# Optimization experiments

Hardware: AMD Instinct MI355X
Metric: run time of the kernel (lower is better)

The kernel has to match this reference:

```python
import jax, jax.numpy as jnp
import numpy as np

B, S, D, H = 4, 2048, 1024, 16
HD = D // H  # head_dim = 64
SCALE = HD ** -0.5


def setup_inputs() -> dict:
    key = jax.random.key(0)
    k1, k2, k3, k4, k5 = jax.random.split(key, 5)
    std = D ** -0.5
    return {
        "x": jax.random.normal(k1, (B, S, D), dtype=jnp.float32),
        "w_qkv": jax.random.normal(k2, (D, 3 * D), dtype=jnp.float32) * std,
        "b_qkv": jax.random.normal(k3, (3 * D,), dtype=jnp.float32) * 0.01,
        "w_out": jax.random.normal(k4, (D, D), dtype=jnp.float32) * std,
        "b_out": jax.random.normal(k5, (D,), dtype=jnp.float32) * 0.01,
    }


def reference(x, w_qkv, b_qkv, w_out, b_out):
    b, s, d = x.shape
    qkv = x @ w_qkv + b_qkv                                   # [B,S,3D]
    qkv = qkv.reshape(b, s, 3, H, HD).transpose(2, 0, 3, 1, 4)  # [3,B,H,S,HD]
    q, k, v = qkv[0], qkv[1], qkv[2]
    attn = jnp.einsum("bhqd,bhkd->bhqk", q, k) * SCALE        # [B,H,S,S]
    attn = jax.nn.softmax(attn, axis=-1)
    out = jnp.einsum("bhqk,bhkd->bhqd", attn, v)              # [B,H,S,HD]
    out = out.transpose(0, 2, 1, 3).reshape(b, s, d)          # [B,S,D]
    return out @ w_out + b_out
```

## Files before the change

kernel.cpp:

```cpp
#include <hip/hip_runtime.h>
#include <stdint.h>
#include <stddef.h>

#define NB 4
#define NS 2048
#define ND 1024
#define NH 16
#define HDIM 64
#define SCALE 0.125f
#define CLOG2E 0.18033688011112042f

typedef __attribute__((ext_vector_type(4))) float f32x4;
typedef __attribute__((ext_vector_type(16))) float f32x16;
typedef __attribute__((ext_vector_type(8))) __bf16 bf16x8;
typedef __attribute__((ext_vector_type(4))) uint32_t u32x4;

__device__ __forceinline__ uint16_t f2bf(float f) {
  uint32_t u = __builtin_bit_cast(uint32_t, f);
  return (uint16_t)((u + 0x7fffu + ((u >> 16) & 1u)) >> 16);
}

__device__ __forceinline__ void gload_lds16(const void* g, void* l) {
  __builtin_amdgcn_global_load_lds((const __attribute__((address_space(1))) void*)g,
                                   (__attribute__((address_space(3))) void*)l, 16, 0, 0);
}

__device__ __forceinline__ uint32_t cvtpk(float lo, float hi) {
  uint32_t r;
  asm("v_cvt_pk_bf16_f32 %0, %1, %2" : "=v"(r) : "v"(lo), "v"(hi));
  return r;
}

__device__ __forceinline__ void permswap(uint32_t& a, uint32_t& b) {
  asm("v_permlane32_swap_b32 %0, %1" : "+v"(a), "+v"(b));
}

__device__ __forceinline__ float fexp2(float x) {
  float r;
  asm("v_exp_f32 %0, %1" : "=v"(r) : "v"(x));
  return r;
}

__global__ __launch_bounds__(256)
void k_prep(const float* __restrict__ x, const float* __restrict__ wq,
            const float* __restrict__ wo, uint16_t* __restrict__ Xb,
            uint16_t* __restrict__ Wq, uint16_t* __restrict__ Wo) {
  __shared__ float tile[64][65];
  const int bid = blockIdx.x, tid = threadIdx.x;
  if (bid < 8192) {
    int i = bid * 256 + tid;
    float4 v = reinterpret_cast<const float4*>(x)[i];
    ushort4 o;
    o.x = f2bf(v.x); o.y = f2bf(v.y); o.z = f2bf(v.z); o.w = f2bf(v.w);
    reinterpret_cast<ushort4*>(Xb)[i] = o;
    return;
  }
  const float* in; uint16_t* out; int K, N, bx, by;
  if (bid < 8960) { int r = bid - 8192; in = wq; out = Wq; K = 1024; N = 3072; bx = r % 48; by = r / 48; }
  else            { int r = bid - 8960; in = wo; out = Wo; K = 1024; N = 1024; bx = r % 16; by = r / 16; }
  const int nb = bx * 64, kb = by * 64;
  const int c = tid & 63, r0 = tid >> 6;
#pragma unroll
  for (int i = 0; i < 16; ++i) {
    int r = r0 * 16 + i;
    tile[r][c] = in[(size_t)(kb + r) * N + nb + c];
  }
  __syncthreads();
#pragma unroll
  for (int i = 0; i < 16; ++i) {
    int rr = r0 * 16 + i;
    out[(size_t)(nb + rr) * K + kb + c] = f2bf(tile[c][rr]);
  }
}

__global__ __launch_bounds__(512)
void k_gemm256(const uint16_t* __restrict__ A, const uint16_t* __restrict__ Bt,
               const float* __restrict__ bias, uint16_t* __restrict__ C,
               uint16_t* __restrict__ vt, int M, int N, int K) {
  __shared__ __align__(16) char Al[2][32768];
  __shared__ __align__(16) char Bl[2][32768];
  const int tid = threadIdx.x, wave = tid >> 6, lane = tid & 63;

  const int flat = blockIdx.y * gridDim.x + blockIdx.x;
  const int cpx = (gridDim.x * gridDim.y) >> 3;
  const int swz = (flat & 7) * cpx + (flat >> 3);
  const int bx = swz % gridDim.x, by = swz / gridDim.x;
  const int mb = by * 256, nb = bx * 256;

  const int wm = wave >> 2, wn = wave & 3;
  const int fr = lane & 15, cc = lane >> 4;
  f32x4 acc[8][4] = {};
  const int NT = K >> 6;
  const int sslot = tid & 7;

#define STAGE(BUF, KT) do {                                                     \
    const int kb_ = (KT) * 64;                                                  \
    _Pragma("unroll")                                                           \
    for (int i = 0; i < 4; ++i) {                                               \
      int row = (i * 512 + tid) >> 3;                                           \
      int ch = sslot ^ (row & 7);                                               \
      gload_lds16(A + (size_t)(mb + row) * K + kb_ + ch * 8,                    \
                  Al[BUF] + (size_t)(i * 512 + (wave << 6)) * 16);              \
    }                                                                           \
    _Pragma("unroll")                                                           \
    for (int i = 0; i < 4; ++i) {                                               \
      int row = (i * 512 + tid) >> 3;                                           \
      int ch = sslot ^ (row & 7);                                               \
      gload_lds16(Bt + (size_t)(nb + row) * K + kb_ + ch * 8,                   \
                  Bl[BUF] + (size_t)(i * 512 + (wave << 6)) * 16);              \
    }                                                                           \
  } while (0)

  STAGE(0, 0);
  asm volatile("s_waitcnt vmcnt(0)" ::: "memory");
  __builtin_amdgcn_s_barrier();

  for (int kt = 0; kt < NT; ++kt) {
    const int cur = kt & 1;
    const bool issue = (kt + 1 < NT);
    if (issue) STAGE(cur ^ 1, kt + 1);

#pragma unroll
    for (int ks = 0; ks < 2; ++ks) {
      bf16x8 af[8], bfg[4];
#pragma unroll
      for (int i = 0; i < 8; ++i) {
        int ra = wm * 128 + i * 16 + fr;
        af[i] = *(const bf16x8*)(Al[cur] + ra * 128 + (((ks * 4 + cc) ^ (ra & 7)) * 16));
      }
#pragma unroll
      for (int j = 0; j < 4; ++j) {
        int rb = wn * 64 + j * 16 + fr;
        bfg[j] = *(const bf16x8*)(Bl[cur] + rb * 128 + (((ks * 4 + cc) ^ (rb & 7)) * 16));
      }
      __builtin_amdgcn_s_setprio(1);
#pragma unroll
      for (int i = 0; i < 8; ++i)
#pragma unroll
        for (int j = 0; j < 4; ++j)
          acc[i][j] = __builtin_amdgcn_mfma_f32_16x16x32_bf16(af[i], bfg[j], acc[i][j], 0, 0, 0);
      __builtin_amdgcn_s_setprio(0);
    }

    if (issue) {
      asm volatile("s_waitcnt vmcnt(0)" ::: "memory");
      __builtin_amdgcn_s_barrier();
    }
  }
#undef STAGE

  if (nb < 2048) {
    const float qs = (nb < 1024) ? CLOG2E : 1.0f;
#pragma unroll
    for (int i = 0; i < 8; ++i)
#pragma unroll
      for (int j = 0; j < 4; ++j)
#pragma unroll
        for (int r = 0; r < 4; ++r) {
          int row = mb + wm * 128 + i * 16 + cc * 4 + r;
          int col = nb + wn * 64 + j * 16 + fr;
          C[(size_t)row * N + col] = f2bf((acc[i][j][r] + bias[col]) * qs);
        }
  } else {
    const int b_ = mb >> 11;
    const int h_ = ((nb - 2048) >> 6) + wn;
    const int s0 = (mb & 2047) + wm * 128;
    uint16_t* vb = vt + (size_t)(b_ * 16 + h_) * 64 * NS;
#pragma unroll
    for (int i = 0; i < 8; ++i)
#pragma unroll
      for (int j = 0; j < 4; ++j) {
        int col = nb + wn * 64 + j * 16 + fr;
        int d = j * 16 + fr;
        float bcol = bias[col];
        ushort4 o;
        o.x = f2bf(acc[i][j][0] + bcol);
        o.y = f2bf(acc[i][j][1] + bcol);
        o.z = f2bf(acc[i][j][2] + bcol);
        o.w = f2bf(acc[i][j][3] + bcol);
        int s = s0 + i * 16 + cc * 4;
        *reinterpret_cast<ushort4*>(vb + (size_t)d * NS + s) = o;
      }
  }
}

template<int OUT_BF16>
__global__ __launch_bounds__(256)
void k_gemm(const uint16_t* __restrict__ A, const uint16_t* __restrict__ Bt,
            const float* __restrict__ bias, void* __restrict__ C,
            int M, int N, int K) {
  __shared__ __align__(16) char Al[8192];
  __shared__ __align__(16) char Bl[8192];
  const int tid = threadIdx.x;
  const int wave = tid >> 6, lane = tid & 63;
  const int mb = blockIdx.y * 128, nb = blockIdx.x * 128;
  const int wm = (wave >> 1) * 64, wn = (wave & 1) * 64;
  const int fr = lane & 15, cc = lane >> 4;
  const int srow = tid >> 2, sch = tid & 3;
  f32x4 acc[4][4] = {};

  for (int kb = 0; kb < K; kb += 32) {
#pragma unroll
    for (int p = 0; p < 2; ++p) {
      int row = p * 64 + srow;
      int cg = sch ^ (row & 3) ^ ((row >> 2) & 3);
      gload_lds16(A + (size_t)(mb + row) * K + kb + cg * 8, Al + p * 4096 + wave * 1024);
      gload_lds16(Bt + (size_t)(nb + row) * K + kb + cg * 8, Bl + p * 4096 + wave * 1024);
    }
    __syncthreads();
    bf16x8 af[4], bfr[4];
#pragma unroll
    for (int i = 0; i < 4; ++i) {
      int ra = wm + i * 16 + fr;
      af[i] = *(const bf16x8*)(Al + ra * 64 + ((cc ^ (ra & 3) ^ ((ra >> 2) & 3)) * 16));
      int rb = wn + i * 16 + fr;
      bfr[i] = *(const bf16x8*)(Bl + rb * 64 + ((cc ^ (rb & 3) ^ ((rb >> 2) & 3)) * 16));
    }
#pragma unroll
    for (int i = 0; i < 4; ++i)
#pragma unroll
      for (int j = 0; j < 4; ++j)
        acc[i][j] = __builtin_amdgcn_mfma_f32_16x16x32_bf16(af[i], bfr[j], acc[i][j], 0, 0, 0);
    __syncthreads();
  }

#pragma unroll
  for (int i = 0; i < 4; ++i)
#pragma unroll
    for (int j = 0; j < 4; ++j)
#pragma unroll
      for (int r = 0; r < 4; ++r) {
        int row = mb + wm + i * 16 + cc * 4 + r;
        int col = nb + wn + j * 16 + fr;
        float v = acc[i][j][r] + bias[col];
        if (OUT_BF16)
          ((uint16_t*)C)[(size_t)row * N + col] = f2bf(v);
        else
          ((float*)C)[(size_t)row * N + col] = v;
      }
}

__global__ __launch_bounds__(256)
void k_attn(const uint16_t* __restrict__ qkv, const uint16_t* __restrict__ vt,
            uint16_t* __restrict__ out) {
  __shared__ __align__(16) char Kl[2][8192];
  __shared__ __align__(16) char Vl[2][8192];

  const int id = blockIdx.y * 16 + blockIdx.x;
  const int wfid = (id & 7) * 128 + (id >> 3);
  const int bh = wfid >> 4, qblk = wfid & 15;
  const int b = bh >> 4, h = bh & 15;
  const int tid = threadIdx.x, wave = tid >> 6, lane = tid & 63;
  const int ln31 = lane & 31, hi = lane >> 5;

  const int q0 = qblk * 128 + wave * 32;
  const uint16_t* qrowp = qkv + (size_t)(b * NS + q0 + ln31) * 3072 + h * 64 + hi * 8;
  bf16x8 qf[4];
#pragma unroll
  for (int kk = 0; kk < 4; ++kk) qf[kk] = *(const bf16x8*)(qrowp + kk * 16);

  const int srow = tid >> 3;
  const int cs = (tid & 7) ^ (srow & 7);
  const uint16_t* ksrc = qkv + (size_t)(b * NS) * 3072 + 1024 + h * 64 + cs * 8;
  const uint16_t* vsrc = vt + (size_t)bh * 64 * NS + cs * 8;

  f32x16 acc0 = {}, acc1 = {};
  float l_run = 0.f;

#pragma unroll
  for (int r = 0; r < 2; ++r) {
    int row = srow + r * 32;
    gload_lds16(ksrc + (size_t)row * 3072, Kl[0] + wave * 1024 + r * 4096);
    gload_lds16(vsrc + (size_t)row * NS, Vl[0] + wave * 1024 + r * 4096);
  }
  asm volatile("s_waitcnt vmcnt(0)" ::: "memory");
  __builtin_amdgcn_s_barrier();
  __builtin_amdgcn_sched_barrier(0);

  const int ksw = ln31 & 7;

  for (int t = 0; t < NS / 64; ++t) {
    const int cur = t & 1;
    if (t < NS / 64 - 1) {
      const int kb2 = (t + 1) * 64;
      char* kd = Kl[cur ^ 1] + wave * 1024;
      char* vd = Vl[cur ^ 1] + wave * 1024;
#pragma unroll
      for (int r = 0; r < 2; ++r) {
        int row = srow + r * 32;
        gload_lds16(ksrc + (size_t)(kb2 + row) * 3072, kd + r * 4096);
        gload_lds16(vsrc + (size_t)row * NS + kb2, vd + r * 4096);
      }
      asm volatile("s_waitcnt vmcnt(4)" ::: "memory");
    } else {
      asm volatile("s_waitcnt vmcnt(0)" ::: "memory");
    }
    __builtin_amdgcn_s_barrier();
    __builtin_amdgcn_sched_barrier(0);

    const char* kb0 = Kl[cur] + ln31 * 128;
    const char* kb1 = kb0 + 32 * 128;
    f32x16 st0 = {}, st1 = {};
    __builtin_amdgcn_s_setprio(1);
#pragma unroll
    for (int kk = 0; kk < 4; ++kk) {
      int c = ((kk * 2 + hi) ^ ksw) * 16;
      bf16x8 k0 = *(const bf16x8*)(kb0 + c);
      bf16x8 k1 = *(const bf16x8*)(kb1 + c);
      st0 = __builtin_amdgcn_mfma_f32_32x32x16_bf16(k0, qf[kk], st0, 0, 0, 0);
      st1 = __builtin_amdgcn_mfma_f32_32x32x16_bf16(k1, qf[kk], st1, 0, 0, 0);
    }
    __builtin_amdgcn_s_setprio(0);

    float rs = 0.f;
#pragma unroll
    for (int r = 0; r < 16; ++r) { st0[r] = fexp2(st0[r]); rs += st0[r]; }
#pragma unroll
    for (int r = 0; r < 16; ++r) { st1[r] = fexp2(st1[r]); rs += st1[r]; }
    l_run += rs;

    const char* vb0 = Vl[cur] + ln31 * 128;
    const char* vb1 = vb0 + 32 * 128;
    __builtin_amdgcn_s_setprio(1);
#pragma unroll
    for (int h2 = 0; h2 < 2; ++h2) {
      f32x16 ph = h2 ? st1 : st0;
#pragma unroll
      for (int s2 = 0; s2 < 2; ++s2) {
        const int kkp = h2 * 2 + s2;
        const int s8 = s2 * 8;
        uint32_t A0 = cvtpk(ph[s8 + 0], ph[s8 + 1]);
        uint32_t A1 = cvtpk(ph[s8 + 2], ph[s8 + 3]);
        uint32_t B0 = cvtpk(ph[s8 + 4], ph[s8 + 5]);
        uint32_t B1 = cvtpk(ph[s8 + 6], ph[s8 + 7]);
        permswap(A0, B0);
        permswap(A1, B1);
        u32x4 pw = {A0, A1, B0, B1};
        bf16x8 pf = __builtin_bit_cast(bf16x8, pw);
        int c = ((kkp * 2 + hi) ^ ksw) * 16;
        bf16x8 v0 = *(const bf16x8*)(vb0 + c);
        bf16x8 v1 = *(const bf16x8*)(vb1 + c);
        acc0 = __builtin_amdgcn_mfma_f32_32x32x16_bf16(v0, pf, acc0, 0, 0, 0);
        acc1 = __builtin_amdgcn_mfma_f32_32x32x16_bf16(v1, pf, acc1, 0, 0, 0);
      }
    }
    __builtin_amdgcn_s_setprio(0);

    __builtin_amdgcn_s_barrier();
  }

  const float rl = 1.0f / (l_run + __shfl_xor(l_run, 32));
  char* sc = (char*)Kl + wave * 4096 + ln31 * 128;
  const int qsw = ln31 & 15;
#pragma unroll
  for (int dn = 0; dn < 2; ++dn) {
    f32x16 a = dn ? acc1 : acc0;
#pragma unroll
    for (int g = 0; g < 4; ++g) {
      uint2 w;
      w.x = cvtpk(a[4 * g + 0] * rl, a[4 * g + 1] * rl);
      w.y = cvtpk(a[4 * g + 2] * rl, a[4 * g + 3] * rl);
      int c8 = (dn * 8 + 2 * g + hi) ^ qsw;
      *(uint2*)(sc + c8 * 8) = w;
    }
  }
  char* outp = (char*)out + ((size_t)(b * NS + q0 + ln31) * 1024 + h * 64 + hi * 32) * 2;
#pragma unroll
  for (int cc2 = 0; cc2 < 4; ++cc2) {
    uint2 va = *(const uint2*)(sc + (((hi * 8 + 2 * cc2 + 0) ^ qsw) * 8));
    uint2 vb2 = *(const uint2*)(sc + (((hi * 8 + 2 * cc2 + 1) ^ qsw) * 8));
    u32x4 o = {va.x, va.y, vb2.x, vb2.y};
    *(u32x4*)(outp + cc2 * 16) = o;
  }
}

extern "C" void kernel_launch(void* const* d_in, const int* in_sizes, int n_in,
                              void* d_out, int out_size, void* d_ws, size_t ws_size,
                              hipStream_t stream) {
  const float* x     = (const float*)d_in[0];
  const float* w_qkv = (const float*)d_in[1];
  const float* b_qkv = (const float*)d_in[2];
  const float* w_out = (const float*)d_in[3];
  const float* b_out = (const float*)d_in[4];
  float* out = (float*)d_out;
  char* ws = (char*)d_ws;

  uint16_t* Xb    = (uint16_t*)(ws);
  uint16_t* Wqkvt = (uint16_t*)(ws + (16u << 20));
  uint16_t* Woutt = (uint16_t*)(ws + (22u << 20));
  uint16_t* QKV   = (uint16_t*)(ws + (24u << 20));
  uint16_t* Vt    = (uint16_t*)(ws + (72u << 20));
  uint16_t* AO    = Xb;

  k_prep<<<9216, 256, 0, stream>>>(x, w_qkv, w_out, Xb, Wqkvt, Woutt);
  k_gemm256<<<dim3(12, 32), 512, 0, stream>>>(Xb, Wqkvt, b_qkv, QKV, Vt, NB * NS, 3 * ND, ND);
  k_attn<<<dim3(16, 64), 256, 0, stream>>>(QKV, Vt, AO);
  k_gemm<0><<<dim3(8, 64), 256, 0, stream>>>(AO, Woutt, b_out, out, NB * NS, ND, ND);
}
```

Measured before the change: 211.2 us.

## Replace 256x256 double-buffered QKV GEMM with simpler 128x128 single-buffer kernel

Swaps the 512-thread 256x256-tile QKV projection GEMM (double-buffered LDS, 64-wide K steps, grid swizzle, setprio) for a 256-thread 128x128-tile kernel with 32-wide K steps, a single LDS buffer and two barriers per iteration. The grid grows from 384 to 1536 blocks, which gives more blocks per CU and lower LDS use. In exchange it loses load/compute overlap inside a block, the L2-friendly swizzle and the per-tile reuse of the larger tile.

After: 223.9 us. +6.0%, slower.

```diff
diff --git a/kernel.cpp b/kernel.cpp
--- a/kernel.cpp
+++ b/kernel.cpp
@@ -73,104 +73,67 @@
   }
 }
 
-__global__ __launch_bounds__(512)
-void k_gemm256(const uint16_t* __restrict__ A, const uint16_t* __restrict__ Bt,
-               const float* __restrict__ bias, uint16_t* __restrict__ C,
-               uint16_t* __restrict__ vt, int M, int N, int K) {
-  __shared__ __align__(16) char Al[2][32768];
-  __shared__ __align__(16) char Bl[2][32768];
-  const int tid = threadIdx.x, wave = tid >> 6, lane = tid & 63;
-
-  const int flat = blockIdx.y * gridDim.x + blockIdx.x;
-  const int cpx = (gridDim.x * gridDim.y) >> 3;
-  const int swz = (flat & 7) * cpx + (flat >> 3);
-  const int bx = swz % gridDim.x, by = swz / gridDim.x;
-  const int mb = by * 256, nb = bx * 256;
-
-  const int wm = wave >> 2, wn = wave & 3;
+__global__ __launch_bounds__(256)
+void k_gemm1(const uint16_t* __restrict__ A, const uint16_t* __restrict__ Bt,
+             const float* __restrict__ bias, uint16_t* __restrict__ C,
+             uint16_t* __restrict__ vt, int M, int N, int K) {
+  __shared__ __align__(16) char Al[8192];
+  __shared__ __align__(16) char Bl[8192];
+  const int tid = threadIdx.x;
+  const int wave = tid >> 6, lane = tid & 63;
+  const int mb = blockIdx.y * 128, nb = blockIdx.x * 128;
+  const int wm = (wave >> 1) * 64, wn = (wave & 1) * 64;
   const int fr = lane & 15, cc = lane >> 4;
-  f32x4 acc[8][4] = {};
-  const int NT = K >> 6;
-  const int sslot = tid & 7;
-
-#define STAGE(BUF, KT) do {                                                     \
-    const int kb_ = (KT) * 64;                                                  \
-    _Pragma("unroll")                                                           \
-    for (int i = 0; i < 4; ++i) {                                               \
-      int row = (i * 512 + tid) >> 3;                                           \
-      int ch = sslot ^ (row & 7);                                               \
-      gload_lds16(A + (size_t)(mb + row) * K + kb_ + ch * 8,                    \
-                  Al[BUF] + (size_t)(i * 512 + (wave << 6)) * 16);              \
-    }                                                                           \
-    _Pragma("unroll")                                                           \
-    for (int i = 0; i < 4; ++i) {                                               \
-      int row = (i * 512 + tid) >> 3;                                           \
-      int ch = sslot ^ (row & 7);                                               \
-      gload_lds16(Bt + (size_t)(nb + row) * K + kb_ + ch * 8,                   \
-                  Bl[BUF] + (size_t)(i * 512 + (wave << 6)) * 16);              \
-    }                                                                           \
-  } while (0)
-
-  STAGE(0, 0);
-  asm volatile("s_waitcnt vmcnt(0)" ::: "memory");
-  __builtin_amdgcn_s_barrier();
-
-  for (int kt = 0; kt < NT; ++kt) {
-    const int cur = kt & 1;
-    const bool issue = (kt + 1 < NT);
-    if (issue) STAGE(cur ^ 1, kt + 1);
-
-#pragma unroll
-    for (int ks = 0; ks < 2; ++ks) {
-      bf16x8 af[8], bfg[4];
-#pragma unroll
-      for (int i = 0; i < 8; ++i) {
-        int ra = wm * 128 + i * 16 + fr;
-        af[i] = *(const bf16x8*)(Al[cur] + ra * 128 + (((ks * 4 + cc) ^ (ra & 7)) * 16));
-      }
-#pragma unroll
-      for (int j = 0; j < 4; ++j) {
-        int rb = wn * 64 + j * 16 + fr;
-        bfg[j] = *(const bf16x8*)(Bl[cur] + rb * 128 + (((ks * 4 + cc) ^ (rb & 7)) * 16));
-      }
-      __builtin_amdgcn_s_setprio(1);
-#pragma unroll
-      for (int i = 0; i < 8; ++i)
-#pragma unroll
-        for (int j = 0; j < 4; ++j)
-          acc[i][j] = __builtin_amdgcn_mfma_f32_16x16x32_bf16(af[i], bfg[j], acc[i][j], 0, 0, 0);
-      __builtin_amdgcn_s_setprio(0);
-    }
-
-    if (issue) {
-      asm volatile("s_waitcnt vmcnt(0)" ::: "memory");
-      __builtin_amdgcn_s_barrier();
-    }
-  }
-#undef STAGE
+  const int srow = tid >> 2, sch = tid & 3;
+  f32x4 acc[4][4] = {};
+
+  for (int kb = 0; kb < K; kb += 32) {
+#pragma unroll
+    for (int p = 0; p < 2; ++p) {
+      int row = p * 64 + srow;
+      int cg = sch ^ (row & 3) ^ ((row >> 2) & 3);
+      gload_lds16(A + (size_t)(mb + row) * K + kb + cg * 8, Al + p * 4096 + wave * 1024);
+      gload_lds16(Bt + (size_t)(nb + row) * K + kb + cg * 8, Bl + p * 4096 + wave * 1024);
+    }
+    __syncthreads();
+    bf16x8 af[4], bfr[4];
+#pragma unroll
+    for (int i = 0; i < 4; ++i) {
+      int ra = wm + i * 16 + fr;
+      af[i] = *(const bf16x8*)(Al + ra * 64 + ((cc ^ (ra & 3) ^ ((ra >> 2) & 3)) * 16));
+      int rb = wn + i * 16 + fr;
+      bfr[i] = *(const bf16x8*)(Bl + rb * 64 + ((cc ^ (rb & 3) ^ ((rb >> 2) & 3)) * 16));
+    }
+#pragma unroll
+    for (int i = 0; i < 4; ++i)
+#pragma unroll
+      for (int j = 0; j < 4; ++j)
+        acc[i][j] = __builtin_amdgcn_mfma_f32_16x16x32_bf16(af[i], bfr[j], acc[i][j], 0, 0, 0);
+    __syncthreads();
+  }
 
   if (nb < 2048) {
     const float qs = (nb < 1024) ? CLOG2E : 1.0f;
 #pragma unroll
-    for (int i = 0; i < 8; ++i)
+    for (int i = 0; i < 4; ++i)
 #pragma unroll
       for (int j = 0; j < 4; ++j)
 #pragma unroll
         for (int r = 0; r < 4; ++r) {
-          int row = mb + wm * 128 + i * 16 + cc * 4 + r;
-          int col = nb + wn * 64 + j * 16 + fr;
+          int row = mb + wm + i * 16 + cc * 4 + r;
+          int col = nb + wn + j * 16 + fr;
           C[(size_t)row * N + col] = f2bf((acc[i][j][r] + bias[col]) * qs);
         }
   } else {
     const int b_ = mb >> 11;
-    const int h_ = ((nb - 2048) >> 6) + wn;
-    const int s0 = (mb & 2047) + wm * 128;
+    const int h_ = ((nb - 2048) >> 6) + (wn >> 6);
+    const int s0 = (mb & 2047) + wm;
     uint16_t* vb = vt + (size_t)(b_ * 16 + h_) * 64 * NS;
 #pragma unroll
-    for (int i = 0; i < 8; ++i)
+    for (int i = 0; i < 4; ++i)
 #pragma unroll
       for (int j = 0; j < 4; ++j) {
-        int col = nb + wn * 64 + j * 16 + fr;
+        int col = nb + wn + j * 16 + fr;
         int d = j * 16 + fr;
         float bcol = bias[col];
         ushort4 o;
@@ -393,7 +356,7 @@
   uint16_t* AO    = Xb;
 
   k_prep<<<9216, 256, 0, stream>>>(x, w_qkv, w_out, Xb, Wqkvt, Woutt);
-  k_gemm256<<<dim3(12, 32), 512, 0, stream>>>(Xb, Wqkvt, b_qkv, QKV, Vt, NB * NS, 3 * ND, ND);
+  k_gemm1<<<dim3(24, 64), 256, 0, stream>>>(Xb, Wqkvt, b_qkv, QKV, Vt, NB * NS, 3 * ND, ND);
   k_attn<<<dim3(16, 64), 256, 0, stream>>>(QKV, Vt, AO);
   k_gemm<0><<<dim3(8, 64), 256, 0, stream>>>(AO, Woutt, b_out, out, NB * NS, ND, ND);
 }
```

## Load V fragments directly from global into registers instead of LDS staging

Applied to the files above, without the earlier changes.

Removes the LDS double buffer for V^T and has each lane load its V fragments for the current tile directly from global memory into registers at the top of each iteration. K staging through LDS is kept, and the vmcnt waits are adjusted to account for the eight extra outstanding vector loads. This cuts LDS traffic and capacity per block, which may raise occupancy. In exchange, each wave now fetches V redundantly, V loads get no prefetch distance beyond the QK^T and softmax phase, and global latency may be exposed.

Result: slower. 252.0 us (+19.3%).

```diff
diff --git a/kernel.cpp b/kernel.cpp
--- a/kernel.cpp
+++ b/kernel.cpp
@@ -244,7 +244,6 @@
 void k_attn(const uint16_t* __restrict__ qkv, const uint16_t* __restrict__ vt,
             uint16_t* __restrict__ out) {
   __shared__ __align__(16) char Kl[2][8192];
-  __shared__ __align__(16) char Vl[2][8192];
 
   const int id = blockIdx.y * 16 + blockIdx.x;
   const int wfid = (id & 7) * 128 + (id >> 3);
@@ -262,17 +261,14 @@
   const int srow = tid >> 3;
   const int cs = (tid & 7) ^ (srow & 7);
   const uint16_t* ksrc = qkv + (size_t)(b * NS) * 3072 + 1024 + h * 64 + cs * 8;
-  const uint16_t* vsrc = vt + (size_t)bh * 64 * NS + cs * 8;
+  const uint16_t* vrow0 = vt + (size_t)bh * 64 * NS + (size_t)ln31 * NS + hi * 8;
+  const uint16_t* vrow1 = vrow0 + (size_t)32 * NS;
 
   f32x16 acc0 = {}, acc1 = {};
   float l_run = 0.f;
 
-#pragma unroll
-  for (int r = 0; r < 2; ++r) {
-    int row = srow + r * 32;
-    gload_lds16(ksrc + (size_t)row * 3072, Kl[0] + wave * 1024 + r * 4096);
-    gload_lds16(vsrc + (size_t)row * NS, Vl[0] + wave * 1024 + r * 4096);
-  }
+  gload_lds16(ksrc + (size_t)srow * 3072, Kl[0] + wave * 1024);
+  gload_lds16(ksrc + (size_t)(srow + 32) * 3072, Kl[0] + wave * 1024 + 4096);
   asm volatile("s_waitcnt vmcnt(0)" ::: "memory");
   __builtin_amdgcn_s_barrier();
   __builtin_amdgcn_sched_barrier(0);
@@ -281,19 +277,22 @@
 
   for (int t = 0; t < NS / 64; ++t) {
     const int cur = t & 1;
+
+    bf16x8 vf0[4], vf1[4];
+#pragma unroll
+    for (int kkp = 0; kkp < 4; ++kkp) {
+      vf0[kkp] = *(const bf16x8*)(vrow0 + t * 64 + kkp * 16);
+      vf1[kkp] = *(const bf16x8*)(vrow1 + t * 64 + kkp * 16);
+    }
+
     if (t < NS / 64 - 1) {
       const int kb2 = (t + 1) * 64;
       char* kd = Kl[cur ^ 1] + wave * 1024;
-      char* vd = Vl[cur ^ 1] + wave * 1024;
-#pragma unroll
-      for (int r = 0; r < 2; ++r) {
-        int row = srow + r * 32;
-        gload_lds16(ksrc + (size_t)(kb2 + row) * 3072, kd + r * 4096);
-        gload_lds16(vsrc + (size_t)row * NS + kb2, vd + r * 4096);
-      }
-      asm volatile("s_waitcnt vmcnt(4)" ::: "memory");
+      gload_lds16(ksrc + (size_t)(kb2 + srow) * 3072, kd);
+      gload_lds16(ksrc + (size_t)(kb2 + srow + 32) * 3072, kd + 4096);
+      asm volatile("s_waitcnt vmcnt(10)" ::: "memory");
     } else {
-      asm volatile("s_waitcnt vmcnt(0)" ::: "memory");
+      asm volatile("s_waitcnt vmcnt(8)" ::: "memory");
     }
     __builtin_amdgcn_s_barrier();
     __builtin_amdgcn_sched_barrier(0);
@@ -319,8 +318,6 @@
     for (int r = 0; r < 16; ++r) { st1[r] = fexp2(st1[r]); rs += st1[r]; }
     l_run += rs;
 
-    const char* vb0 = Vl[cur] + ln31 * 128;
-    const char* vb1 = vb0 + 32 * 128;
     __builtin_amdgcn_s_setprio(1);
 #pragma unroll
     for (int h2 = 0; h2 < 2; ++h2) {
@@ -337,11 +334,8 @@
         permswap(A1, B1);
         u32x4 pw = {A0, A1, B0, B1};
         bf16x8 pf = __builtin_bit_cast(bf16x8, pw);
-        int c = ((kkp * 2 + hi) ^ ksw) * 16;
-        bf16x8 v0 = *(const bf16x8*)(vb0 + c);
-        bf16x8 v1 = *(const bf16x8*)(vb1 + c);
-        acc0 = __builtin_amdgcn_mfma_f32_32x32x16_bf16(v0, pf, acc0, 0, 0, 0);
-        acc1 = __builtin_amdgcn_mfma_f32_32x32x16_bf16(v1, pf, acc1, 0, 0, 0);
+        acc0 = __builtin_amdgcn_mfma_f32_32x32x16_bf16(vf0[kkp], pf, acc0, 0, 0, 0);
+        acc1 = __builtin_amdgcn_mfma_f32_32x32x16_bf16(vf1[kkp], pf, acc1, 0, 0, 0);
       }
     }
     __builtin_amdgcn_s_setprio(0);
```
